# Kernel optimization log

Hardware: AMD Instinct MI355X
Metric: run time of the kernel (lower is better)

Reference implementation:

```python
import jax, jax.numpy as jnp
import numpy as np

D = 1024   # hidden
H = 4      # heads
HD = D // H
E = 8      # experts
FF = 4096  # expert ffn dim
CAP_FACTOR = 1.0


def _ln(x, g, b, eps=1e-5):
    mu = jnp.mean(x, -1, keepdims=True)
    v = jnp.mean((x - mu) ** 2, -1, keepdims=True)
    return (x - mu) * jax.lax.rsqrt(v + eps) * g + b


def setup_inputs() -> dict:
    key = jax.random.key(0)
    ks = jax.random.split(key, 8)
    L, N = 1024, 16
    s = 0.02
    return {
        "x": jax.random.normal(ks[0], (L, N, D), jnp.float32),
        "in_proj_w": jax.random.normal(ks[1], (3 * D, D), jnp.float32) * s,
        "in_proj_b": jnp.zeros((3 * D,), jnp.float32),
        "out_proj_w": jax.random.normal(ks[2], (D, D), jnp.float32) * s,
        "out_proj_b": jnp.zeros((D,), jnp.float32),
        "ln1_g": jnp.ones((D,), jnp.float32),
        "ln1_b": jnp.zeros((D,), jnp.float32),
        "ln2_g": jnp.ones((D,), jnp.float32),
        "ln2_b": jnp.zeros((D,), jnp.float32),
        "wg": jax.random.normal(ks[3], (D, E), jnp.float32) * s,
        "w1": jax.random.normal(ks[4], (E, D, FF), jnp.float32) * s,
        "b1": jnp.zeros((E, FF), jnp.float32),
        "w2": jax.random.normal(ks[5], (E, FF, D), jnp.float32) * s,
        "b2": jnp.zeros((E, D), jnp.float32),
    }


def _mha(x, w, b, ow, ob):
    # x: [L, N, D] (torch MultiheadAttention layout, batch_first=False)
    L, N, _ = x.shape
    qkv = x @ w.T + b
    q, k, v = jnp.split(qkv, 3, axis=-1)
    rh = lambda t: t.reshape(L, N, H, HD).transpose(1, 2, 0, 3)  # -> [N,H,L,HD]
    q, k, v = rh(q), rh(k), rh(v)
    scores = jnp.einsum('nhld,nhmd->nhlm', q, k) / np.float32(np.sqrt(HD))
    attn = jax.nn.softmax(scores, axis=-1)
    o = jnp.einsum('nhlm,nhmd->nhld', attn, v).transpose(2, 0, 1, 3).reshape(L, N, D)
    return o @ ow.T + ob


def _moe(x, wg, w1, b1, w2, b2):
    # top-1 switch gating with capacity drop, dispatch, grouped GEMM, combine
    L, N, _ = x.shape
    S = L * N
    cap = int(CAP_FACTOR * S) // E  # 2048
    xf = x.reshape(S, D)
    gates = jax.nn.softmax(xf @ wg, axis=-1)           # [S,E]
    idx = jnp.argmax(gates, axis=-1)                    # [S] top-1 expert
    mask1 = jax.nn.one_hot(idx, E, dtype=x.dtype)       # [S,E]
    # position of each token within its expert's queue
    loc = jnp.sum((jnp.cumsum(mask1, 0) - 1.0) * mask1, -1).astype(jnp.int32)
    keep = loc < cap                                    # capacity drop mask
    gate_val = jnp.take_along_axis(gates, idx[:, None], -1)[:, 0]
    slot = jnp.where(keep, idx.astype(jnp.int32) * cap + loc, E * cap)  # OOB if dropped
    disp = jnp.zeros((E * cap, D), x.dtype).at[slot].set(xf, mode='drop')
    disp = disp.reshape(E, cap, D)
    # expert = Linear(D,FF) -> Linear(FF,D), NO activation between (per source)
    h = jnp.einsum('ecd,edf->ecf', disp, w1) + b1[:, None, :]
    y = (jnp.einsum('ecf,efd->ecd', h, w2) + b2[:, None, :]).reshape(E * cap, D)
    out = jnp.where(keep[:, None], gate_val[:, None] * y[jnp.minimum(slot, E * cap - 1)], 0.0)
    return out.reshape(L, N, D)


def reference(x, in_proj_w, in_proj_b, out_proj_w, out_proj_b,
              ln1_g, ln1_b, ln2_g, ln2_b, wg, w1, b1, w2, b2):
    y1 = _ln(x + _mha(x, in_proj_w, in_proj_b, out_proj_w, out_proj_b), ln1_g, ln1_b)
    y2 = _ln(y1 + _moe(y1, wg, w1, b1, w2, b2), ln2_g, ln2_b)
    return y2
```

## Files before the change

kernel.cpp:

```cpp
#include <hip/hip_runtime.h>
#include <hip/hip_bf16.h>

typedef __bf16 bf16_t;
typedef bf16_t bf16x8 __attribute__((ext_vector_type(8)));
typedef float  f32x4  __attribute__((ext_vector_type(4)));
typedef _Float16 half4 __attribute__((ext_vector_type(4)));
typedef _Float16 half8 __attribute__((ext_vector_type(8)));

#define L_  1024
#define N_  16
#define S_  16384
#define D_  1024
#define H_  4
#define HD_ 256
#define E_  8
#define FF_ 4096
#define CAP_ 2048
#define ESLOTS_ (E_*CAP_)

__device__ __forceinline__ void gload16(const void* g, void* l) {
  __builtin_amdgcn_global_load_lds(
      (const __attribute__((address_space(1))) void*)g,
      (__attribute__((address_space(3))) void*)l,
      16, 0, 0);
}

__global__ __launch_bounds__(256) void split2(
    const float* __restrict__ in, _Float16* __restrict__ oh,
    _Float16* __restrict__ ol, long n4)
{
  long i = (long)blockIdx.x * blockDim.x + threadIdx.x;
  long stride = (long)gridDim.x * blockDim.x;
  for (; i < n4; i += stride) {
    float4 v = ((const float4*)in)[i];
    half4 h, l;
    h.x = (_Float16)v.x; l.x = (_Float16)((v.x - (float)h.x) * 4096.0f);
    h.y = (_Float16)v.y; l.y = (_Float16)((v.y - (float)h.y) * 4096.0f);
    h.z = (_Float16)v.z; l.z = (_Float16)((v.z - (float)h.z) * 4096.0f);
    h.w = (_Float16)v.w; l.w = (_Float16)((v.w - (float)h.w) * 4096.0f);
    ((half4*)oh)[i] = h;
    ((half4*)ol)[i] = l;
  }
}

template<int EPI, bool HAS_BIAS>
__global__ __launch_bounds__(256) void hgemm3s(
    const _Float16* __restrict__ Ah, const _Float16* __restrict__ Al,
    const _Float16* __restrict__ Bh, const _Float16* __restrict__ Bl,
    float* __restrict__ Cf, _Float16* __restrict__ Ch, _Float16* __restrict__ Cl,
    const float* __restrict__ bias,
    int K, long lda, long ldb, long ldcf, long ldch,
    int Z2, long sA1, long sA2, long sB1, long sB2, long sC1, long sC2, long sBias)
{
  __shared__ _Float16 tA[2][128 * 32];
  __shared__ _Float16 tB[2][64 * 32];
  const int z  = blockIdx.z;
  const int z1 = z / Z2, z2 = z - z1 * Z2;
  const long aoff = (long)z1 * sA1 + (long)z2 * sA2;
  const long boff = (long)z1 * sB1 + (long)z2 * sB2;
  const long coff = (long)z1 * sC1 + (long)z2 * sC2;
  const int brow = blockIdx.x * 128, bcol = blockIdx.y * 64;
  const int tid = threadIdx.x, lane = tid & 63, wid = tid >> 6;
  const int wr = (wid >> 1) * 64, wc = (wid & 1) * 32;
  const int fr = lane & 15, fq = (lane >> 4) * 8;

  const _Float16* sbA = ((wid == 0) ? Ah : Al) + aoff
                        + (long)(brow + (lane >> 2)) * lda + (lane & 3) * 8;
  const _Float16* sbB = ((wid == 2) ? Bh : Bl) + boff
                        + (long)(bcol + (lane >> 2)) * ldb + (lane & 3) * 8;

  f32x4 acc0[4][2], acc1[4][2];
#pragma unroll
  for (int mi = 0; mi < 4; ++mi)
#pragma unroll
    for (int ni = 0; ni < 2; ++ni) {
      acc0[mi][ni] = f32x4{0.f, 0.f, 0.f, 0.f};
      acc1[mi][ni] = f32x4{0.f, 0.f, 0.f, 0.f};
    }

  for (int k0 = 0; k0 < K; k0 += 32) {
    if (wid < 2) {
#pragma unroll
      for (int i = 0; i < 8; ++i)
        gload16(sbA + (long)(16 * i) * lda + k0, &tA[wid][i * 512]);
    } else {
#pragma unroll
      for (int i = 0; i < 4; ++i)
        gload16(sbB + (long)(16 * i) * ldb + k0, &tB[wid - 2][i * 512]);
    }
    __syncthreads();

    half8 bh_[2], bl_[2];
#pragma unroll
    for (int ni = 0; ni < 2; ++ni) {
      bh_[ni] = *(const half8*)&tB[0][(wc + ni * 16 + fr) * 32 + fq];
      bl_[ni] = *(const half8*)&tB[1][(wc + ni * 16 + fr) * 32 + fq];
    }
    half8 ah_[4], al_[4];
#pragma unroll
    for (int mi = 0; mi < 4; ++mi) {
      ah_[mi] = *(const half8*)&tA[0][(wr + mi * 16 + fr) * 32 + fq];
      al_[mi] = *(const half8*)&tA[1][(wr + mi * 16 + fr) * 32 + fq];
    }
#pragma unroll
    for (int mi = 0; mi < 4; ++mi)
#pragma unroll
      for (int ni = 0; ni < 2; ++ni)
        acc0[mi][ni] = __builtin_amdgcn_mfma_f32_16x16x32_f16(ah_[mi], bh_[ni], acc0[mi][ni], 0, 0, 0);
#pragma unroll
    for (int mi = 0; mi < 4; ++mi)
#pragma unroll
      for (int ni = 0; ni < 2; ++ni)
        acc1[mi][ni] = __builtin_amdgcn_mfma_f32_16x16x32_f16(ah_[mi], bl_[ni], acc1[mi][ni], 0, 0, 0);
#pragma unroll
    for (int mi = 0; mi < 4; ++mi)
#pragma unroll
      for (int ni = 0; ni < 2; ++ni)
        acc1[mi][ni] = __builtin_amdgcn_mfma_f32_16x16x32_f16(al_[mi], bh_[ni], acc1[mi][ni], 0, 0, 0);
    __syncthreads();
  }

#pragma unroll
  for (int mi = 0; mi < 4; ++mi) {
#pragma unroll
    for (int ni = 0; ni < 2; ++ni) {
      int gcol = bcol + wc + ni * 16 + fr;
      float bv = 0.0f;
      if constexpr (HAS_BIAS) bv = bias[(long)z1 * sBias + gcol];
#pragma unroll
      for (int v = 0; v < 4; ++v) {
        int grow = brow + wr + mi * 16 + (lane >> 4) * 4 + v;
        float val = acc0[mi][ni][v] + acc1[mi][ni][v] * 0.000244140625f + bv;
        if constexpr (EPI == 0) {
          Cf[coff + (long)grow * ldcf + gcol] = val;
        } else if constexpr (EPI == 1) {
          _Float16 hh = (_Float16)val;
          _Float16 ll = (_Float16)((val - (float)hh) * 4096.0f);
          long ci = coff + (long)grow * ldch + gcol;
          Ch[ci] = hh; Cl[ci] = ll;
        } else {
          if (bcol < 2048) {
            _Float16 hh = (_Float16)val;
            _Float16 ll = (_Float16)((val - (float)hh) * 4096.0f);
            long ci = (long)grow * ldch + gcol;
            Ch[ci] = hh; Cl[ci] = ll;
          } else {
            Cf[(long)grow * ldcf + (gcol - 2048)] = val;
          }
        }
      }
    }
  }
}

template<bool OUT_BF16, bool HAS_BIAS>
__global__ __launch_bounds__(256) void bgemm16(
    const bf16_t* __restrict__ A, const bf16_t* __restrict__ B,
    void* __restrict__ Cout, const float* __restrict__ bias,
    int K, long lda, long ldb, long ldc,
    long sA1, long sB1, long sC1, long sBias)
{
  __shared__ bf16_t tiles[2][128 * 32];
  const int z = blockIdx.z;
  const long coff = (long)z * sC1;
  const int brow = blockIdx.x * 128, bcol = blockIdx.y * 128;
  const int tid = threadIdx.x, lane = tid & 63, wid = tid >> 6;
  const int wr = (wid >> 1) * 64, wc = (wid & 1) * 64;
  const int fr = lane & 15, fq = (lane >> 4) * 8;

  const bf16_t* src0 = (wid < 2) ? (A + (long)z * sA1) : (B + (long)z * sB1);
  const long ld = (wid < 2) ? lda : ldb;
  const int  rb = ((wid < 2) ? brow : bcol) + 64 * (wid & 1) + (lane >> 2);
  const bf16_t* srcbase = src0 + (long)rb * ld + (lane & 3) * 8;
  const int t = wid >> 1, halfsel = wid & 1;

  f32x4 acc[4][4];
#pragma unroll
  for (int mi = 0; mi < 4; ++mi)
#pragma unroll
    for (int ni = 0; ni < 4; ++ni)
      acc[mi][ni] = f32x4{0.0f, 0.0f, 0.0f, 0.0f};

  for (int k0 = 0; k0 < K; k0 += 32) {
#pragma unroll
    for (int i = 0; i < 4; ++i)
      gload16(srcbase + (long)(16 * i) * ld + k0, &tiles[t][(4 * halfsel + i) * 512]);
    __syncthreads();

    bf16x8 af[4], bfv[4];
#pragma unroll
    for (int i = 0; i < 4; ++i) {
      af[i]  = *(const bf16x8*)&tiles[0][(wr + i * 16 + fr) * 32 + fq];
      bfv[i] = *(const bf16x8*)&tiles[1][(wc + i * 16 + fr) * 32 + fq];
    }
#pragma unroll
    for (int mi = 0; mi < 4; ++mi)
#pragma unroll
      for (int ni = 0; ni < 4; ++ni)
        acc[mi][ni] = __builtin_amdgcn_mfma_f32_16x16x32_bf16(af[mi], bfv[ni], acc[mi][ni], 0, 0, 0);
    __syncthreads();
  }

#pragma unroll
  for (int mi = 0; mi < 4; ++mi) {
#pragma unroll
    for (int ni = 0; ni < 4; ++ni) {
      int gcol = bcol + wc + ni * 16 + fr;
      float bv = 0.0f;
      if constexpr (HAS_BIAS) bv = bias[(long)z * sBias + gcol];
#pragma unroll
      for (int v = 0; v < 4; ++v) {
        int grow = brow + wr + mi * 16 + (lane >> 4) * 4 + v;
        float val = acc[mi][ni][v] + bv;
        long ci = coff + (long)grow * ldc + gcol;
        if constexpr (OUT_BF16) ((bf16_t*)Cout)[ci] = (bf16_t)val;
        else                    ((float*)Cout)[ci]  = val;
      }
    }
  }
}

template<typename TOUT>
__global__ __launch_bounds__(256) void transpose_f32(
    const float* __restrict__ src, TOUT* __restrict__ dst,
    long ld_src, long ld_dst, int Z2,
    long ss1, long ss2, long sd1, long sd2)
{
  __shared__ float t[32][33];
  const int z = blockIdx.z, z1 = z / Z2, z2 = z - z1 * Z2;
  src += (long)z1 * ss1 + (long)z2 * ss2;
  dst += (long)z1 * sd1 + (long)z2 * sd2;
  const int c0 = blockIdx.x * 32, r0 = blockIdx.y * 32;
  const int tx = threadIdx.x & 31, ty = threadIdx.x >> 5;
#pragma unroll
  for (int i = 0; i < 4; ++i)
    t[ty + i * 8][tx] = src[(long)(r0 + ty + i * 8) * ld_src + c0 + tx];
  __syncthreads();
#pragma unroll
  for (int i = 0; i < 4; ++i)
    dst[(long)(c0 + ty + i * 8) * ld_dst + r0 + tx] = (TOUT)t[tx][ty + i * 8];
}

__global__ __launch_bounds__(256) void transpose_split(
    const float* __restrict__ src, _Float16* __restrict__ dh, _Float16* __restrict__ dl,
    long ld_src, long ld_dst, int Z2,
    long ss1, long ss2, long sd1, long sd2)
{
  __shared__ float t[32][33];
  const int z = blockIdx.z, z1 = z / Z2, z2 = z - z1 * Z2;
  src += (long)z1 * ss1 + (long)z2 * ss2;
  dh  += (long)z1 * sd1 + (long)z2 * sd2;
  dl  += (long)z1 * sd1 + (long)z2 * sd2;
  const int c0 = blockIdx.x * 32, r0 = blockIdx.y * 32;
  const int tx = threadIdx.x & 31, ty = threadIdx.x >> 5;
#pragma unroll
  for (int i = 0; i < 4; ++i)
    t[ty + i * 8][tx] = src[(long)(r0 + ty + i * 8) * ld_src + c0 + tx];
  __syncthreads();
#pragma unroll
  for (int i = 0; i < 4; ++i) {
    float v = t[tx][ty + i * 8];
    _Float16 h = (_Float16)v;
    _Float16 l = (_Float16)((v - (float)h) * 4096.0f);
    long idx = (long)(c0 + ty + i * 8) * ld_dst + r0 + tx;
    dh[idx] = h;
    dl[idx] = l;
  }
}

__global__ __launch_bounds__(256) void softmax_inplace_split(
    float* __restrict__ Sm, float scale)
{
  __shared__ float red[4];
  const long row = blockIdx.x;
  const float4* p = (const float4*)(Sm + row * 1024);
  const int tid = threadIdx.x;
  float4 v = p[tid];
  float m = fmaxf(fmaxf(v.x, v.y), fmaxf(v.z, v.w));
#pragma unroll
  for (int o = 32; o; o >>= 1) m = fmaxf(m, __shfl_xor(m, o, 64));
  if ((tid & 63) == 0) red[tid >> 6] = m;
  __syncthreads();
  m = fmaxf(fmaxf(red[0], red[1]), fmaxf(red[2], red[3]));
  __syncthreads();
  float e0 = __expf((v.x - m) * scale);
  float e1 = __expf((v.y - m) * scale);
  float e2 = __expf((v.z - m) * scale);
  float e3 = __expf((v.w - m) * scale);
  float s = e0 + e1 + e2 + e3;
#pragma unroll
  for (int o = 32; o; o >>= 1) s += __shfl_xor(s, o, 64);
  if ((tid & 63) == 0) red[tid >> 6] = s;
  __syncthreads();
  s = red[0] + red[1] + red[2] + red[3];
  float inv = 1.0f / s;
  float p0 = e0 * inv, p1 = e1 * inv, p2 = e2 * inv, p3 = e3 * inv;
  half4 h, l;
  h.x = (_Float16)p0; l.x = (_Float16)((p0 - (float)h.x) * 4096.0f);
  h.y = (_Float16)p1; l.y = (_Float16)((p1 - (float)h.y) * 4096.0f);
  h.z = (_Float16)p2; l.z = (_Float16)((p2 - (float)h.z) * 4096.0f);
  h.w = (_Float16)p3; l.w = (_Float16)((p3 - (float)h.w) * 4096.0f);
  _Float16* base = (_Float16*)Sm + row * 2048;
  ((half4*)base)[tid] = h;
  ((half4*)(base + 1024))[tid] = l;
}

__global__ __launch_bounds__(256) void add_ln(
    const float* __restrict__ a, const float* __restrict__ b,
    const float* __restrict__ g, const float* __restrict__ be,
    float* __restrict__ y, bf16_t* __restrict__ yb)
{
  __shared__ float red[4];
  const long s = blockIdx.x;
  const int tid = threadIdx.x;
  const int lane = tid & 63, w = tid >> 6;
  float4 va = ((const float4*)(a + s * 1024))[tid];
  float4 vb = ((const float4*)(b + s * 1024))[tid];
  float v0 = va.x + vb.x, v1 = va.y + vb.y, v2 = va.z + vb.z, v3 = va.w + vb.w;
  float sum = v0 + v1 + v2 + v3;
#pragma unroll
  for (int o = 32; o; o >>= 1) sum += __shfl_xor(sum, o, 64);
  if (lane == 0) red[w] = sum;
  __syncthreads();
  float mu = (red[0] + red[1] + red[2] + red[3]) * (1.0f / 1024.0f);
  __syncthreads();
  float d0 = v0 - mu, d1 = v1 - mu, d2 = v2 - mu, d3 = v3 - mu;
  float ss = d0 * d0 + d1 * d1 + d2 * d2 + d3 * d3;
#pragma unroll
  for (int o = 32; o; o >>= 1) ss += __shfl_xor(ss, o, 64);
  if (lane == 0) red[w] = ss;
  __syncthreads();
  float var = (red[0] + red[1] + red[2] + red[3]) * (1.0f / 1024.0f);
  float rstd = rsqrtf(var + 1e-5f);
  float4 vg  = ((const float4*)g)[tid];
  float4 vbe = ((const float4*)be)[tid];
  float o0 = d0 * rstd * vg.x + vbe.x;
  float o1 = d1 * rstd * vg.y + vbe.y;
  float o2 = d2 * rstd * vg.z + vbe.z;
  float o3 = d3 * rstd * vg.w + vbe.w;
  float4 ov = {o0, o1, o2, o3};
  ((float4*)(y + s * 1024))[tid] = ov;
  bf16_t* yp = yb + s * 1024 + tid * 4;
  yp[0] = (bf16_t)o0; yp[1] = (bf16_t)o1; yp[2] = (bf16_t)o2; yp[3] = (bf16_t)o3;
}

__global__ __launch_bounds__(256) void combine_ln(
    const float* __restrict__ y1, const float* __restrict__ ymoe,
    const int* __restrict__ slot, const float* __restrict__ gval,
    const float* __restrict__ g, const float* __restrict__ be,
    float* __restrict__ out)
{
  __shared__ float red[4];
  const long s = blockIdx.x;
  const int tid = threadIdx.x;
  const int lane = tid & 63, w = tid >> 6;
  int sl = slot[s];
  bool keep = sl < ESLOTS_;
  float gv = keep ? gval[s] : 0.0f;
  long mrow = keep ? (long)sl * 1024 : 0;
  float4 va = ((const float4*)(y1 + s * 1024))[tid];
  float4 vm = ((const float4*)(ymoe + mrow))[tid];
  float v0 = va.x + gv * vm.x, v1 = va.y + gv * vm.y;
  float v2 = va.z + gv * vm.z, v3 = va.w + gv * vm.w;
  float sum = v0 + v1 + v2 + v3;
#pragma unroll
  for (int o = 32; o; o >>= 1) sum += __shfl_xor(sum, o, 64);
  if (lane == 0) red[w] = sum;
  __syncthreads();
  float mu = (red[0] + red[1] + red[2] + red[3]) * (1.0f / 1024.0f);
  __syncthreads();
  float d0 = v0 - mu, d1 = v1 - mu, d2 = v2 - mu, d3 = v3 - mu;
  float ss = d0 * d0 + d1 * d1 + d2 * d2 + d3 * d3;
#pragma unroll
  for (int o = 32; o; o >>= 1) ss += __shfl_xor(ss, o, 64);
  if (lane == 0) red[w] = ss;
  __syncthreads();
  float var = (red[0] + red[1] + red[2] + red[3]) * (1.0f / 1024.0f);
  float rstd = rsqrtf(var + 1e-5f);
  float4 vg  = ((const float4*)g)[tid];
  float4 vbe = ((const float4*)be)[tid];
  float4 ov = {d0 * rstd * vg.x + vbe.x, d1 * rstd * vg.y + vbe.y,
               d2 * rstd * vg.z + vbe.z, d3 * rstd * vg.w + vbe.w};
  ((float4*)(out + s * 1024))[tid] = ov;
}

__global__ __launch_bounds__(256) void gate_topk(
    const float* __restrict__ y1, const float* __restrict__ wg,
    int* __restrict__ idx, float* __restrict__ gval)
{
  __shared__ float wgs[8 * 1024];
  const int tid = threadIdx.x;
  for (int j = tid; j < 8192; j += 256)
    wgs[(j & 7) * 1024 + (j >> 3)] = wg[j];
  __syncthreads();
  const int lane = tid & 63, w = tid >> 6;
  const long s = (long)blockIdx.x * 4 + w;
  const float* xr = y1 + s * 1024;
  float acc[8] = {0, 0, 0, 0, 0, 0, 0, 0};
  for (int i = 0; i < 16; ++i) {
    int d = lane + i * 64;
    float xv = xr[d];
#pragma unroll
    for (int e = 0; e < 8; ++e) acc[e] = fmaf(xv, wgs[e * 1024 + d], acc[e]);
  }
#pragma unroll
  for (int e = 0; e < 8; ++e) {
#pragma unroll
    for (int o = 32; o; o >>= 1) acc[e] += __shfl_xor(acc[e], o, 64);
  }
  if (lane == 0) {
    float best = acc[0]; int bi = 0;
#pragma unroll
    for (int e = 1; e < 8; ++e) { if (acc[e] > best) { best = acc[e]; bi = e; } }
    float sum = 0.0f;
#pragma unroll
    for (int e = 0; e < 8; ++e) sum += __expf(acc[e] - best);
    idx[s] = bi;
    gval[s] = 1.0f / sum;
  }
}

__global__ __launch_bounds__(1024) void route_scan(
    const int* __restrict__ idx, int* __restrict__ slot, int* __restrict__ tfs)
{
  __shared__ int c_lds[8][1024];
  const int tid = threadIdx.x;
  const int lane = tid & 63, wid = tid >> 6;

  for (int j = tid; j < ESLOTS_; j += 1024) tfs[j] = -1;

  int myc[8] = {0, 0, 0, 0, 0, 0, 0, 0};
  for (int j = 0; j < 16; ++j) {
    int e = idx[tid * 16 + j];
    myc[e]++;
  }
#pragma unroll
  for (int e = 0; e < 8; ++e) c_lds[e][tid] = myc[e];
  __syncthreads();

  if (wid < 8) {
    int carry = 0;
    for (int cb = 0; cb < 1024; cb += 64) {
      int v = c_lds[wid][cb + lane];
#pragma unroll
      for (int o = 1; o < 64; o <<= 1) {
        int t = __shfl_up(v, o, 64);
        if (lane >= o) v += t;
      }
      v += carry;
      c_lds[wid][cb + lane] = v;
      carry = __shfl(v, 63, 64);
    }
  }
  __syncthreads();

  int run[8] = {0, 0, 0, 0, 0, 0, 0, 0};
  for (int j = 0; j < 16; ++j) {
    int s = tid * 16 + j;
    int e = idx[s];
    int excl = c_lds[e][tid] - myc[e];
    int loc = excl + run[e];
    run[e]++;
    int sl = (loc < CAP_) ? e * CAP_ + loc : ESLOTS_;
    slot[s] = sl;
    if (sl < ESLOTS_) tfs[sl] = s;
  }
}

__global__ void dispatch_rows(
    const int* __restrict__ tfs, const bf16_t* __restrict__ y1b,
    bf16_t* __restrict__ disp)
{
  const int row = blockIdx.x;
  const int t = tfs[row];
  bf16x8* d = (bf16x8*)(disp + (long)row * 1024);
  if (t >= 0) {
    const bf16x8* sp = (const bf16x8*)(y1b + (long)t * 1024);
    d[threadIdx.x] = sp[threadIdx.x];
  } else {
    bf16x8 zv;
#pragma unroll
    for (int i = 0; i < 8; ++i) zv[i] = (bf16_t)0.0f;
    d[threadIdx.x] = zv;
  }
}

__global__ void fill_val(float* __restrict__ p, float v, long n)
{
  long i = (long)blockIdx.x * blockDim.x + threadIdx.x;
  long stride = (long)gridDim.x * blockDim.x;
  for (; i < n; i += stride) p[i] = v;
}

extern "C" void kernel_launch(void* const* d_in, const int* in_sizes, int n_in,
                              void* d_out, int out_size, void* d_ws, size_t ws_size,
                              hipStream_t stream)
{
  const float* x    = (const float*)d_in[0];
  const float* Wqkv = (const float*)d_in[1];
  const float* bqkv = (const float*)d_in[2];
  const float* Wo   = (const float*)d_in[3];
  const float* bo   = (const float*)d_in[4];
  const float* g1   = (const float*)d_in[5];
  const float* b1n  = (const float*)d_in[6];
  const float* g2   = (const float*)d_in[7];
  const float* b2n  = (const float*)d_in[8];
  const float* wg   = (const float*)d_in[9];
  const float* w1   = (const float*)d_in[10];
  const float* b1e  = (const float*)d_in[11];
  const float* w2   = (const float*)d_in[12];
  const float* b2e  = (const float*)d_in[13];
  float* out = (float*)d_out;

  const size_t MB = 1ull << 20;
  const size_t REQUIRED = 384 * MB;
  if (ws_size < REQUIRED) {
    fill_val<<<2048, 256, 0, stream>>>(out, (float)(ws_size >> 20), (long)out_size);
    return;
  }

  char* ws = (char*)d_ws;
  _Float16* Xh   = (_Float16*)(ws + 0);
  _Float16* Xl   = (_Float16*)(ws + 32 * MB);
  _Float16* Wqh  = (_Float16*)(ws + 64 * MB);
  _Float16* Wql  = (_Float16*)(ws + 70 * MB);
  float*    scores = (float*)(ws + 0);
  _Float16* Woh  = (_Float16*)(ws + 64 * MB);
  _Float16* Wol  = (_Float16*)(ws + 66 * MB);
  _Float16* QKh  = (_Float16*)(ws + 80 * MB);
  _Float16* QKl  = (_Float16*)(ws + 144 * MB);
  float*    Vf32 = (float*)(ws + 208 * MB);
  _Float16* oh   = (_Float16*)(ws + 208 * MB);
  _Float16* ol   = (_Float16*)(ws + 240 * MB);
  _Float16* vTh  = (_Float16*)(ws + 272 * MB);
  _Float16* vTl  = (_Float16*)(ws + 304 * MB);
  float*    attn = (float*)(ws + 0);
  float*    y1   = (float*)(ws + 80 * MB);
  bf16_t*   y1b  = (bf16_t*)(ws + 144 * MB);
  bf16_t*   disp = (bf16_t*)(ws + 176 * MB);
  int*      idx  = (int*)(ws + 336 * MB);
  int*      slot = idx + S_;
  float*    gval = (float*)(slot + S_);
  int*      tfs  = (int*)(gval + S_);
  bf16_t*   W1t  = (bf16_t*)(ws + 0);
  bf16_t*   W2t  = (bf16_t*)(ws + 0);
  bf16_t*   h    = (bf16_t*)(ws + 208 * MB);
  float*    ymoe = (float*)(ws + 144 * MB);

  split2<<<4096, 256, 0, stream>>>(x, Xh, Xl, (long)S_ * D_ / 4);
  split2<<<2048, 256, 0, stream>>>(Wqkv, Wqh, Wql, (long)3 * D_ * D_ / 4);

  hgemm3s<2, true><<<dim3(128, 48, 1), 256, 0, stream>>>(
      Xh, Xl, Wqh, Wql, Vf32, QKh, QKl, bqkv,
      D_, D_, D_, D_, 2 * D_,
      1, 0, 0, 0, 0, 0, 0, 0);

  split2<<<1024, 256, 0, stream>>>(Wo, Woh, Wol, (long)D_ * D_ / 4);

  transpose_split<<<dim3(HD_ / 32, L_ / 32, 64), 256, 0, stream>>>(
      Vf32, vTh, vTl, (long)N_ * D_, L_,
      H_, D_, HD_, (long)H_ * HD_ * L_, (long)HD_ * L_);

  for (int g = 0; g < 4; ++g) {
    const long qko = (long)g * 4 * 2048;
    hgemm3s<0, false><<<dim3(8, 16, 16), 256, 0, stream>>>(
        QKh + qko, QKl + qko, QKh + qko + 1024, QKl + qko + 1024,
        scores, nullptr, nullptr, nullptr,
        HD_, (long)N_ * 2048, (long)N_ * 2048, L_, 0,
        H_, 2048, 256, 2048, 256, (long)H_ * L_ * L_, (long)L_ * L_, 0);
    softmax_inplace_split<<<4 * H_ * L_, 256, 0, stream>>>(scores, 0.0625f);
    hgemm3s<1, false><<<dim3(8, 4, 16), 256, 0, stream>>>(
        (_Float16*)scores, (_Float16*)scores + 1024,
        vTh + (long)g * 4 * H_ * HD_ * L_, vTl + (long)g * 4 * H_ * HD_ * L_,
        nullptr, oh + (long)g * 4 * D_, ol + (long)g * 4 * D_, nullptr,
        L_, 2048, L_, 0, (long)N_ * D_,
        H_, (long)4 * L_ * 2048, (long)L_ * 2048,
        (long)H_ * HD_ * L_, (long)HD_ * L_, D_, HD_, 0);
  }

  hgemm3s<0, true><<<dim3(128, 16, 1), 256, 0, stream>>>(
      oh, ol, Woh, Wol, attn, nullptr, nullptr, bo,
      D_, D_, D_, D_, 0,
      1, 0, 0, 0, 0, 0, 0, 0);

  add_ln<<<S_, 256, 0, stream>>>(x, attn, g1, b1n, y1, y1b);

  gate_topk<<<S_ / 4, 256, 0, stream>>>(y1, wg, idx, gval);

  route_scan<<<1, 1024, 0, stream>>>(idx, slot, tfs);

  dispatch_rows<<<ESLOTS_, 128, 0, stream>>>(tfs, y1b, disp);

  transpose_f32<bf16_t><<<dim3(FF_ / 32, D_ / 32, E_), 256, 0, stream>>>(
      w1, W1t, FF_, D_, 1, (long)D_ * FF_, 0, (long)FF_ * D_, 0);

  bgemm16<true, true><<<dim3(16, 32, 8), 256, 0, stream>>>(
      disp, W1t, h, b1e, D_, D_, D_, FF_,
      (long)CAP_ * D_, (long)FF_ * D_, (long)CAP_ * FF_, FF_);

  transpose_f32<bf16_t><<<dim3(D_ / 32, FF_ / 32, E_), 256, 0, stream>>>(
      w2, W2t, D_, FF_, 1, (long)FF_ * D_, 0, (long)D_ * FF_, 0);

  bgemm16<false, true><<<dim3(16, 8, 8), 256, 0, stream>>>(
      h, W2t, ymoe, b2e, FF_, FF_, FF_, D_,
      (long)CAP_ * FF_, (long)D_ * FF_, (long)CAP_ * D_, D_);

  combine_ln<<<S_, 256, 0, stream>>>(y1, ymoe, slot, gval, g2, b2n, out);
}
```

Before: 1.753 ms.

## Double-buffer LDS tiles in fp16-split and bf16 GEMM main loops

Both GEMM kernels (the three-pass fp16 hi/lo split GEMM and the bf16 GEMM) now keep two LDS stages. The first K-tile is loaded before the loop, and each iteration issues the global-to-LDS loads for the next tile before computing on the current one. This drops one barrier per iteration and is meant to overlap the direct-to-LDS global loads with the MFMA work, hiding memory latency. In exchange LDS use per block doubles, which can lower how many blocks fit on each compute unit.

```diff
diff --git a/kernel.cpp b/kernel.cpp
--- a/kernel.cpp
+++ b/kernel.cpp
@@ -52,8 +52,8 @@
     int K, long lda, long ldb, long ldcf, long ldch,
     int Z2, long sA1, long sA2, long sB1, long sB2, long sC1, long sC2, long sBias)
 {
-  __shared__ _Float16 tA[2][128 * 32];
-  __shared__ _Float16 tB[2][64 * 32];
+  __shared__ _Float16 tA[2][2][128 * 32];
+  __shared__ _Float16 tB[2][2][64 * 32];
   const int z  = blockIdx.z;
   const int z1 = z / Z2, z2 = z - z1 * Z2;
   const long aoff = (long)z1 * sA1 + (long)z2 * sA2;
@@ -68,6 +68,7 @@
                         + (long)(brow + (lane >> 2)) * lda + (lane & 3) * 8;
   const _Float16* sbB = ((wid == 2) ? Bh : Bl) + boff
                         + (long)(bcol + (lane >> 2)) * ldb + (lane & 3) * 8;
+  const int limbsel = wid & 1;
 
   f32x4 acc0[4][2], acc1[4][2];
 #pragma unroll
@@ -78,29 +79,44 @@
       acc1[mi][ni] = f32x4{0.f, 0.f, 0.f, 0.f};
     }
 
-  for (int k0 = 0; k0 < K; k0 += 32) {
-    if (wid < 2) {
-#pragma unroll
-      for (int i = 0; i < 8; ++i)
-        gload16(sbA + (long)(16 * i) * lda + k0, &tA[wid][i * 512]);
-    } else {
-#pragma unroll
-      for (int i = 0; i < 4; ++i)
-        gload16(sbB + (long)(16 * i) * ldb + k0, &tB[wid - 2][i * 512]);
-    }
-    __syncthreads();
+  if (wid < 2) {
+#pragma unroll
+    for (int i = 0; i < 8; ++i)
+      gload16(sbA + (long)(16 * i) * lda, &tA[limbsel][0][i * 512]);
+  } else {
+#pragma unroll
+    for (int i = 0; i < 4; ++i)
+      gload16(sbB + (long)(16 * i) * ldb, &tB[limbsel][0][i * 512]);
+  }
+  __syncthreads();
+
+  const int NT = K >> 5;
+  for (int t = 0; t < NT; ++t) {
+    const int cur = t & 1;
+    if (t + 1 < NT) {
+      const int k1 = (t + 1) * 32;
+      if (wid < 2) {
+#pragma unroll
+        for (int i = 0; i < 8; ++i)
+          gload16(sbA + (long)(16 * i) * lda + k1, &tA[limbsel][cur ^ 1][i * 512]);
+      } else {
+#pragma unroll
+        for (int i = 0; i < 4; ++i)
+          gload16(sbB + (long)(16 * i) * ldb + k1, &tB[limbsel][cur ^ 1][i * 512]);
+      }
+    }
 
     half8 bh_[2], bl_[2];
 #pragma unroll
     for (int ni = 0; ni < 2; ++ni) {
-      bh_[ni] = *(const half8*)&tB[0][(wc + ni * 16 + fr) * 32 + fq];
-      bl_[ni] = *(const half8*)&tB[1][(wc + ni * 16 + fr) * 32 + fq];
+      bh_[ni] = *(const half8*)&tB[0][cur][(wc + ni * 16 + fr) * 32 + fq];
+      bl_[ni] = *(const half8*)&tB[1][cur][(wc + ni * 16 + fr) * 32 + fq];
     }
     half8 ah_[4], al_[4];
 #pragma unroll
     for (int mi = 0; mi < 4; ++mi) {
-      ah_[mi] = *(const half8*)&tA[0][(wr + mi * 16 + fr) * 32 + fq];
-      al_[mi] = *(const half8*)&tA[1][(wr + mi * 16 + fr) * 32 + fq];
+      ah_[mi] = *(const half8*)&tA[0][cur][(wr + mi * 16 + fr) * 32 + fq];
+      al_[mi] = *(const half8*)&tA[1][cur][(wr + mi * 16 + fr) * 32 + fq];
     }
 #pragma unroll
     for (int mi = 0; mi < 4; ++mi)
@@ -160,7 +176,7 @@
     int K, long lda, long ldb, long ldc,
     long sA1, long sB1, long sC1, long sBias)
 {
-  __shared__ bf16_t tiles[2][128 * 32];
+  __shared__ bf16_t tiles[2][2][128 * 32];
   const int z = blockIdx.z;
   const long coff = (long)z * sC1;
   const int brow = blockIdx.x * 128, bcol = blockIdx.y * 128;
@@ -172,7 +188,7 @@
   const long ld = (wid < 2) ? lda : ldb;
   const int  rb = ((wid < 2) ? brow : bcol) + 64 * (wid & 1) + (lane >> 2);
   const bf16_t* srcbase = src0 + (long)rb * ld + (lane & 3) * 8;
-  const int t = wid >> 1, halfsel = wid & 1;
+  const int tsel = wid >> 1, halfsel = wid & 1;
 
   f32x4 acc[4][4];
 #pragma unroll
@@ -181,17 +197,26 @@
     for (int ni = 0; ni < 4; ++ni)
       acc[mi][ni] = f32x4{0.0f, 0.0f, 0.0f, 0.0f};
 
-  for (int k0 = 0; k0 < K; k0 += 32) {
-#pragma unroll
-    for (int i = 0; i < 4; ++i)
-      gload16(srcbase + (long)(16 * i) * ld + k0, &tiles[t][(4 * halfsel + i) * 512]);
-    __syncthreads();
+#pragma unroll
+  for (int i = 0; i < 4; ++i)
+    gload16(srcbase + (long)(16 * i) * ld, &tiles[tsel][0][(4 * halfsel + i) * 512]);
+  __syncthreads();
+
+  const int NT = K >> 5;
+  for (int t = 0; t < NT; ++t) {
+    const int cur = t & 1;
+    if (t + 1 < NT) {
+      const int k1 = (t + 1) * 32;
+#pragma unroll
+      for (int i = 0; i < 4; ++i)
+        gload16(srcbase + (long)(16 * i) * ld + k1, &tiles[tsel][cur ^ 1][(4 * halfsel + i) * 512]);
+    }
 
     bf16x8 af[4], bfv[4];
 #pragma unroll
     for (int i = 0; i < 4; ++i) {
-      af[i]  = *(const bf16x8*)&tiles[0][(wr + i * 16 + fr) * 32 + fq];
-      bfv[i] = *(const bf16x8*)&tiles[1][(wc + i * 16 + fr) * 32 + fq];
+      af[i]  = *(const bf16x8*)&tiles[0][cur][(wr + i * 16 + fr) * 32 + fq];
+      bfv[i] = *(const bf16x8*)&tiles[1][cur][(wc + i * 16 + fr) * 32 + fq];
     }
 #pragma unroll
     for (int mi = 0; mi < 4; ++mi)
```

After: 1.686 ms. 3.8% less time.
